# Optimization experiments

Measured on AMD Instinct MI355X. Metric: run time of the kernel, lower is better.

The kernel has to match this reference:

```python
import jax, jax.numpy as jnp
import numpy as np

T, B, S, H, E, V = 16, 32, 256, 256, 300, 1000


def setup_inputs() -> dict:
    key = jax.random.key(0)
    ks = jax.random.split(key, 16)
    p = lambda k, shp: (jax.random.normal(k, shp, dtype=jnp.float32) * 0.05)
    return {
        "target_variable": jax.random.randint(ks[0], (T, B), 0, V),
        "h0": p(ks[1], (1, B, H)),
        "c0": p(ks[2], (1, B, H)),
        "encoder_outputs": jax.random.normal(ks[3], (S, B, H), dtype=jnp.float32),
        "encoder_lens": jax.random.randint(ks[4], (B,), 1, S + 1),
        "embedding": p(ks[5], (V, E)),
        "W_ih": p(ks[6], (4 * H, E)),
        "W_hh": p(ks[7], (4 * H, H)),
        "b_ih": p(ks[8], (4 * H,)),
        "b_hh": p(ks[9], (4 * H,)),
        "We": p(ks[10], (H, H)),
        "be": p(ks[11], (H,)),
        "Wd": p(ks[12], (H, H)),
        "bd": p(ks[13], (H,)),
        "wa": p(ks[14], (H,)),
        "ba": p(ks[14], (1,)),
        "W_out": p(ks[15], (V, 2 * H)),
        "b_out": p(ks[15], (V,)),
    }


def _lstm(x, h0, c0, W_ih, W_hh, b_ih, b_hh):
    # x: [T,B,E]; torch gate order i,f,g,o
    x_proj = jnp.einsum('tbe,ge->tbg', x, W_ih) + b_ih  # [T,B,4H]
    def step(carry, xg):
        h, c = carry
        g = xg + h @ W_hh.T + b_hh
        i, f, gg, o = jnp.split(g, 4, axis=-1)
        c = jax.nn.sigmoid(f) * c + jax.nn.sigmoid(i) * jnp.tanh(gg)
        h = jax.nn.sigmoid(o) * jnp.tanh(c)
        return (h, c), h
    (hT, cT), outs = jax.lax.scan(step, (h0[0], c0[0]), x_proj)
    return outs, hT[None], cT[None]


def reference(target_variable, h0, c0, encoder_outputs, encoder_lens,
              embedding, W_ih, W_hh, b_ih, b_hh,
              We, be, Wd, bd, wa, ba, W_out, b_out):
    emb = embedding[target_variable]                      # [T,B,E] (dropout p=0 -> identity)
    output, hT, cT = _lstm(emb, h0, c0, W_ih, W_hh, b_ih, b_hh)  # output [T,B,H]
    # additive attention: same math as expand+Linear, applied before broadcast
    enc_t = jnp.einsum('sbh,gh->sbg', encoder_outputs, We) + be   # [S,B,H]
    dec_t = jnp.einsum('tbh,gh->tbg', output, Wd) + bd            # [T,B,H]
    scores = jnp.einsum('tsbh,h->tsb', jnp.tanh(enc_t[None, :, :, :] + dec_t[:, None, :, :]), wa) + ba[0]
    raw_attention = jnp.transpose(scores, (2, 0, 1))              # [B,T,S]
    valid = (jnp.arange(S)[None, None, :] < encoder_lens[:, None, None])  # [B,1,S]
    raw_attention = jnp.where(valid, raw_attention, -jnp.inf)
    attention = jax.nn.softmax(raw_attention, axis=2)             # [B,T,S]
    enc_bf = jnp.transpose(encoder_outputs, (1, 0, 2))            # [B,S,H]
    context = jnp.einsum('bts,bsh->bth', attention, enc_bf)       # [B,T,H]
    out_bf = jnp.transpose(output, (1, 0, 2))                     # [B,T,H]
    combined = jnp.transpose(jnp.concatenate([context, out_bf], axis=2), (1, 0, 2))  # [T,B,2H]
    logits = jnp.einsum('tbh,vh->tbv', combined, W_out) + b_out
    output_prob = jax.nn.softmax(logits, axis=2)                  # [T,B,V]
    return output_prob, hT, cT, context
```

## Files before the change

kernel.cpp:

```cpp
#include <hip/hip_runtime.h>
#include <hip/hip_fp16.h>
#include <math.h>

typedef unsigned int u32;
typedef unsigned short u16;

#define T_ 16
#define B_ 32
#define S_ 256
#define H_ 256
#define E_ 300
#define V_ 1000

typedef _Float16 h2_t __attribute__((ext_vector_type(2)));
typedef __fp16  fp16v2 __attribute__((ext_vector_type(2)));

__device__ __forceinline__ float fast_tanh(float x) {
    return 1.0f - 2.0f / (__expf(2.0f * x) + 1.0f);
}
__device__ __forceinline__ float fast_sigm(float x) {
    return 1.0f / (1.0f + __expf(-x));
}
__device__ __forceinline__ float bf2f(u16 x) { return __uint_as_float(((u32)x) << 16); }
__device__ __forceinline__ float blo(u32 u) { return __uint_as_float(u << 16); }
__device__ __forceinline__ float bhi(u32 u) { return __uint_as_float(u & 0xffff0000u); }
__device__ __forceinline__ u16 f2bf(float f) {
    u32 u = __float_as_uint(f);
    u32 r = (u + 0x7fffu + ((u >> 16) & 1u)) >> 16;
    return (u16)r;
}
__device__ __forceinline__ h2_t u2h2(u32 u) {
    union { u32 a; h2_t b; } c; c.a = u; return c.b;
}
__device__ __forceinline__ u32 pk2(float a, float b) {
    union { fp16v2 v; u32 u; } c; c.v = __builtin_amdgcn_cvt_pkrtz(a, b); return c.u;
}
__device__ __forceinline__ float dot2f16(u32 w, u32 h, float acc) {
#if __has_builtin(__builtin_amdgcn_fdot2)
    return __builtin_amdgcn_fdot2(u2h2(w), u2h2(h), acc, false);
#else
    h2_t wv = u2h2(w), hv = u2h2(h);
    return acc + (float)wv.x * (float)hv.x + (float)wv.y * (float)hv.y;
#endif
}

__device__ void gemm_tile_256(const float* __restrict__ A, const int* __restrict__ gidx,
                              int lda, const float* __restrict__ Bw,
                              const float* __restrict__ bias, float* __restrict__ C,
                              int N, int K, int ldc, int bm, int bn)
{
    __shared__ float As[32][64];
    __shared__ float Bs[32][64];
    const int tid = threadIdx.x;
    const int ty = tid >> 4, tx = tid & 15;
    const int lr = tid >> 2;
    const int lk = (tid & 3) * 8;

    int am = bm + lr;
    int arow = gidx ? gidx[am] : am;
    const float* Ap = A + (size_t)arow * lda;
    int bnr = bn + lr;
    const float* Bp = (bnr < N) ? (Bw + (size_t)bnr * K) : nullptr;

    float acc[4][4] = {};

    for (int k0 = 0; k0 < K; k0 += 32) {
        int kb = k0 + lk;
        float av[8];
        if (kb + 8 <= K) {
            float4 p0 = *(const float4*)(Ap + kb);
            float4 p1 = *(const float4*)(Ap + kb + 4);
            av[0]=p0.x; av[1]=p0.y; av[2]=p0.z; av[3]=p0.w;
            av[4]=p1.x; av[5]=p1.y; av[6]=p1.z; av[7]=p1.w;
        } else {
            #pragma unroll
            for (int j = 0; j < 8; j++) av[j] = (kb + j < K) ? Ap[kb + j] : 0.0f;
        }
        #pragma unroll
        for (int j = 0; j < 8; j++) As[lk + j][lr] = av[j];
        if (Bp && kb + 8 <= K) {
            float4 p0 = *(const float4*)(Bp + kb);
            float4 p1 = *(const float4*)(Bp + kb + 4);
            av[0]=p0.x; av[1]=p0.y; av[2]=p0.z; av[3]=p0.w;
            av[4]=p1.x; av[5]=p1.y; av[6]=p1.z; av[7]=p1.w;
        } else if (Bp) {
            #pragma unroll
            for (int j = 0; j < 8; j++) av[j] = (kb + j < K) ? Bp[kb + j] : 0.0f;
        } else {
            #pragma unroll
            for (int j = 0; j < 8; j++) av[j] = 0.0f;
        }
        #pragma unroll
        for (int j = 0; j < 8; j++) Bs[lk + j][lr] = av[j];
        __syncthreads();
        #pragma unroll
        for (int kk = 0; kk < 32; kk++) {
            float4 a = *(const float4*)&As[kk][ty * 4];
            float4 b = *(const float4*)&Bs[kk][tx * 4];
            acc[0][0] += a.x*b.x; acc[0][1] += a.x*b.y; acc[0][2] += a.x*b.z; acc[0][3] += a.x*b.w;
            acc[1][0] += a.y*b.x; acc[1][1] += a.y*b.y; acc[1][2] += a.y*b.z; acc[1][3] += a.y*b.w;
            acc[2][0] += a.z*b.x; acc[2][1] += a.z*b.y; acc[2][2] += a.z*b.z; acc[2][3] += a.z*b.w;
            acc[3][0] += a.w*b.x; acc[3][1] += a.w*b.y; acc[3][2] += a.w*b.z; acc[3][3] += a.w*b.w;
        }
        __syncthreads();
    }
    #pragma unroll
    for (int i = 0; i < 4; i++) {
        int m = bm + ty * 4 + i;
        #pragma unroll
        for (int j = 0; j < 4; j++) {
            int n = bn + tx * 4 + j;
            if (n < N) C[(size_t)m * ldc + n] = acc[i][j] + bias[n];
        }
    }
}

__global__ __launch_bounds__(256)
void prep_xproj(const float* __restrict__ emb, const int* __restrict__ tv,
                const float* __restrict__ W_ih, const float* __restrict__ b_ih,
                float* __restrict__ xproj,
                const float* __restrict__ Whh,  u32* __restrict__ Wt2,
                const float* __restrict__ Wd,   float* __restrict__ Wdt,
                const float* __restrict__ W_out, u16* __restrict__ WoTb)
{
    const int bid = blockIdx.x;
    if (bid < 128) {
        gemm_tile_256(emb, tv, E_, W_ih, b_ih, xproj, 1024, E_, 1024,
                      (bid >> 4) * 64, (bid & 15) * 64);
        return;
    }
    __shared__ float tile[64][65];
    const int tid = threadIdx.x;
    const int wv = tid >> 6;
    const int lane = tid & 63;

    if (bid < 192) {
        int t = bid - 128;
        int r0 = (t >> 2) * 64, k0 = (t & 3) * 64;
        #pragma unroll 4
        for (int j = 0; j < 16; j++) {
            int row = wv * 16 + j;
            tile[row][lane] = Whh[(size_t)(r0 + row) * 256 + k0 + lane];
        }
        __syncthreads();
        #pragma unroll
        for (int it = 0; it < 2; it++) {
            int q = wv + 4 * it;
            uint4 val;
            val.x = pk2(tile[lane][8*q + 0], tile[lane][8*q + 1]);
            val.y = pk2(tile[lane][8*q + 2], tile[lane][8*q + 3]);
            val.z = pk2(tile[lane][8*q + 4], tile[lane][8*q + 5]);
            val.w = pk2(tile[lane][8*q + 6], tile[lane][8*q + 7]);
            ((uint4*)Wt2)[(size_t)((k0 >> 3) + q) * 1024 + r0 + lane] = val;
        }
    } else if (bid < 208) {
        int t = bid - 192;
        int h0 = (t >> 2) * 64, k0 = (t & 3) * 64;
        #pragma unroll 4
        for (int j = 0; j < 16; j++) {
            int row = wv * 16 + j;
            tile[row][lane] = Wd[(size_t)(h0 + row) * 256 + k0 + lane];
        }
        __syncthreads();
        #pragma unroll
        for (int it = 0; it < 4; it++) {
            int q = wv + 4 * it;
            float4 v;
            v.x = tile[lane][4*q + 0];
            v.y = tile[lane][4*q + 1];
            v.z = tile[lane][4*q + 2];
            v.w = tile[lane][4*q + 3];
            ((float4*)Wdt)[(size_t)((k0 >> 2) + q) * 256 + h0 + lane] = v;
        }
    } else {
        int t = bid - 208;
        int v0 = (t >> 3) * 64, k0 = (t & 7) * 64;
        #pragma unroll 4
        for (int j = 0; j < 16; j++) {
            int row = wv * 16 + j;
            int v = v0 + row;
            tile[row][lane] = (v < V_) ? W_out[(size_t)v * 512 + k0 + lane] : 0.0f;
        }
        __syncthreads();
        #pragma unroll
        for (int it = 0; it < 4; it++) {
            int q = wv + 4 * it;
            int v = v0 + lane;
            float a0 = tile[lane][4*q + 0], a1 = tile[lane][4*q + 1];
            float a2 = tile[lane][4*q + 2], a3 = tile[lane][4*q + 3];
            float b0 = __shfl_xor(a0, 1, 64), b1 = __shfl_xor(a1, 1, 64);
            float b2 = __shfl_xor(a2, 1, 64), b3 = __shfl_xor(a3, 1, 64);
            if (!(lane & 1) && v < V_) {
                uint4 w;
                w.x = (u32)f2bf(a0) | ((u32)f2bf(b0) << 16);
                w.y = (u32)f2bf(a1) | ((u32)f2bf(b1) << 16);
                w.z = (u32)f2bf(a2) | ((u32)f2bf(b2) << 16);
                w.w = (u32)f2bf(a3) | ((u32)f2bf(b3) << 16);
                ((uint4*)WoTb)[(size_t)((k0 >> 2) + q) * 500 + (v >> 1)] = w;
            }
        }
    }
}

__global__ __launch_bounds__(1024, 4)
void lstm_enct(const float* __restrict__ xproj,
               const u32*   __restrict__ Wt2,
               const float* __restrict__ bhh,
               const float* __restrict__ h0, const float* __restrict__ c0,
               float* __restrict__ combined,
               float* __restrict__ hT, float* __restrict__ cT,
               const float* __restrict__ enc_raw,
               const float* __restrict__ We,
               const float* __restrict__ be,
               float* __restrict__ enct)
{
    const int bid = blockIdx.x;
    const int tid = threadIdx.x;
    __shared__ __align__(16) u32 smem[34176];

    if (bid < 32) {
        float* zs = (float*)smem;
        float* cs = (float*)(smem + 1024);
        u32*   hp = smem + 1280;
        u32*   wlds = smem + 1408;
        const int b = bid;
        const int r = tid;
        if (tid < 256) {
            float h0v = h0[b * 256 + tid];
            cs[tid] = c0[b * 256 + tid];
            float hpart = __shfl_xor(h0v, 1, 64);
            if (!(tid & 1)) hp[tid >> 1] = pk2(h0v, hpart);
        }
        const float bh = bhh[r];
        const uint4* wp4 = (const uint4*)Wt2 + r;

        uint4 wreg[16];
        #pragma unroll
        for (int j = 0; j < 16; j++) wreg[j] = wp4[(size_t)(16 + j) * 1024];
        #pragma unroll
        for (int j = 0; j < 8; j++) {
            uint4 w = wp4[(size_t)(8 + j) * 1024];
            wlds[(j * 4 + 0) * 1024 + r] = w.x;
            wlds[(j * 4 + 1) * 1024 + r] = w.y;
            wlds[(j * 4 + 2) * 1024 + r] = w.z;
            wlds[(j * 4 + 3) * 1024 + r] = w.w;
        }
        __syncthreads();

        for (int t = 0; t < T_; t++) {
            float xp = xproj[((size_t)t * B_ + b) * 1024 + r];
            float acc = 0.0f;
            const uint4* hp4 = (const uint4*)hp;
            #pragma unroll
            for (int i = 0; i < 8; i++) {
                uint4 hv = hp4[i];
                uint4 w  = wp4[(size_t)i * 1024];
                acc = dot2f16(w.x, hv.x, acc);
                acc = dot2f16(w.y, hv.y, acc);
                acc = dot2f16(w.z, hv.z, acc);
                acc = dot2f16(w.w, hv.w, acc);
            }
            #pragma unroll
            for (int j = 0; j < 8; j++) {
                uint4 hv = hp4[8 + j];
                u32 w0 = wlds[(j * 4 + 0) * 1024 + r];
                u32 w1 = wlds[(j * 4 + 1) * 1024 + r];
                u32 w2 = wlds[(j * 4 + 2) * 1024 + r];
                u32 w3 = wlds[(j * 4 + 3) * 1024 + r];
                acc = dot2f16(w0, hv.x, acc);
                acc = dot2f16(w1, hv.y, acc);
                acc = dot2f16(w2, hv.z, acc);
                acc = dot2f16(w3, hv.w, acc);
            }
            #pragma unroll
            for (int j = 0; j < 16; j++) {
                uint4 hv = hp4[16 + j];
                acc = dot2f16(wreg[j].x, hv.x, acc);
                acc = dot2f16(wreg[j].y, hv.y, acc);
                acc = dot2f16(wreg[j].z, hv.z, acc);
                acc = dot2f16(wreg[j].w, hv.w, acc);
            }
            zs[r] = xp + bh + acc;
            __syncthreads();

            if (tid < 256) {
                float ig = fast_sigm(zs[tid]);
                float fg = fast_sigm(zs[256 + tid]);
                float gg = fast_tanh(zs[512 + tid]);
                float og = fast_sigm(zs[768 + tid]);
                float c = fg * cs[tid] + ig * gg;
                float h = og * fast_tanh(c);
                cs[tid] = c;
                combined[((size_t)t * B_ + b) * 512 + 256 + tid] = h;
                if (t == T_ - 1) {
                    hT[b * 256 + tid] = h;
                    cT[b * 256 + tid] = c;
                }
                float hpart = __shfl_xor(h, 1, 64);
                if (!(tid & 1)) hp[tid >> 1] = pk2(h, hpart);
            }
            __syncthreads();
        }
    } else {
        float (*As2)[132] = (float (*)[132])smem;
        float (*Bs2)[132] = (float (*)[132])(smem + 4224);
        const int tile = bid - 32;
        const int bm = (tile >> 1) * 128;
        const int bn = (tile & 1) * 128;
        const int tx = tid & 31, ty = tid >> 5;
        const int lr = tid >> 3;
        const int lk = (tid & 7) * 4;

        const float* Ap = enc_raw + (size_t)(bm + lr) * 256;
        const float* Bp = We + (size_t)(bn + lr) * 256;
        float acc[4][4] = {};

        for (int k0 = 0; k0 < 256; k0 += 32) {
            float4 a4 = *(const float4*)(Ap + k0 + lk);
            float4 b4 = *(const float4*)(Bp + k0 + lk);
            As2[lk + 0][lr] = a4.x; As2[lk + 1][lr] = a4.y;
            As2[lk + 2][lr] = a4.z; As2[lk + 3][lr] = a4.w;
            Bs2[lk + 0][lr] = b4.x; Bs2[lk + 1][lr] = b4.y;
            Bs2[lk + 2][lr] = b4.z; Bs2[lk + 3][lr] = b4.w;
            __syncthreads();
            #pragma unroll
            for (int kk = 0; kk < 32; kk++) {
                float4 a = *(const float4*)&As2[kk][ty * 4];
                float4 b = *(const float4*)&Bs2[kk][tx * 4];
                acc[0][0] += a.x*b.x; acc[0][1] += a.x*b.y; acc[0][2] += a.x*b.z; acc[0][3] += a.x*b.w;
                acc[1][0] += a.y*b.x; acc[1][1] += a.y*b.y; acc[1][2] += a.y*b.z; acc[1][3] += a.y*b.w;
                acc[2][0] += a.z*b.x; acc[2][1] += a.z*b.y; acc[2][2] += a.z*b.z; acc[2][3] += a.z*b.w;
                acc[3][0] += a.w*b.x; acc[3][1] += a.w*b.y; acc[3][2] += a.w*b.z; acc[3][3] += a.w*b.w;
            }
            __syncthreads();
        }
        #pragma unroll
        for (int i = 0; i < 4; i++) {
            int m = bm + ty * 4 + i;
            #pragma unroll
            for (int j = 0; j < 4; j++) {
                int n = bn + tx * 4 + j;
                enct[(size_t)m * 256 + n] = acc[i][j] + be[n];
            }
        }
    }
}

__global__ __launch_bounds__(512)
void attn_logits(const float* __restrict__ enct,
                 const float* __restrict__ combined_in,
                 const float* __restrict__ Wdt,
                 const float* __restrict__ bd,
                 const float* __restrict__ enc_raw,
                 const float* __restrict__ wa, const float* __restrict__ ba,
                 const int* __restrict__ lens,
                 const u16* __restrict__ WoTb,
                 const float* __restrict__ b_out,
                 float* __restrict__ ctx_out,
                 float* __restrict__ probs)
{
    const int bid = blockIdx.x;
    const int b = bid & 31;
    const int t = bid >> 5;
    const int tid = threadIdx.x;
    const int wv = tid >> 6, lane = tid & 63;
    __shared__ float ds[256], was[256], sc[256];
    __shared__ float crow[512];
    __shared__ float tmp2[512];
    __shared__ float lrow[1000];
    __shared__ float red[8], red2[8];

    if (tid < 256) {
        crow[256 + tid] = combined_in[((size_t)t * B_ + b) * 512 + 256 + tid];
        was[tid] = wa[tid];
    }
    const int len = lens[b];
    const float bav = ba[0];
    __syncthreads();

    {
        const int h   = tid & 255;
        const int kq0 = (tid >> 8) * 32;
        float acc = 0.0f;
        const float4* wp = (const float4*)Wdt + h;
        #pragma unroll 8
        for (int kq = kq0; kq < kq0 + 32; kq++) {
            float4 w = wp[(size_t)kq * 256];
            float4 c = *(const float4*)&crow[256 + kq * 4];
            acc += w.x * c.x;
            acc += w.y * c.y;
            acc += w.z * c.z;
            acc += w.w * c.w;
        }
        tmp2[tid] = acc;
    }
    __syncthreads();
    if (tid < 256) ds[tid] = bd[tid] + tmp2[tid] + tmp2[tid + 256];
    __syncthreads();

    for (int s = wv; s < len; s += 8) {
        const float* er = enct + ((size_t)s * B_ + b) * 256;
        float sum = 0.0f;
        #pragma unroll
        for (int j = 0; j < 4; j++) {
            int h = lane + 64 * j;
            sum += fast_tanh(er[h] + ds[h]) * was[h];
        }
        #pragma unroll
        for (int off = 32; off >= 1; off >>= 1) sum += __shfl_xor(sum, off, 64);
        if (lane == 0) sc[s] = sum + bav;
    }
    __syncthreads();

    float x = (tid < len) ? sc[tid] : -INFINITY;
    float m = x;
    #pragma unroll
    for (int off = 32; off >= 1; off >>= 1) m = fmaxf(m, __shfl_xor(m, off, 64));
    if (lane == 0) red[wv] = m;
    __syncthreads();
    m = red[0];
    #pragma unroll
    for (int i = 1; i < 8; i++) m = fmaxf(m, red[i]);
    float e = __expf(x - m);
    float ssum = e;
    #pragma unroll
    for (int off = 32; off >= 1; off >>= 1) ssum += __shfl_xor(ssum, off, 64);
    if (lane == 0) red2[wv] = ssum;
    __syncthreads();
    ssum = red2[0] + red2[1] + red2[2] + red2[3] + red2[4] + red2[5] + red2[6] + red2[7];
    if (tid < 256) sc[tid] = e / ssum;
    __syncthreads();

    {
        const int h  = tid & 255;
        const int sg = tid >> 8;
        const int mid = (len + 1) >> 1;
        const int s0 = sg ? mid : 0;
        const int s1 = sg ? len : mid;
        float cacc = 0.0f;
        const float* eb = enc_raw + (size_t)b * 256 + h;
        #pragma unroll 4
        for (int s = s0; s < s1; s++) cacc += sc[s] * eb[(size_t)s * (B_ * H_)];
        tmp2[tid] = cacc;
    }
    __syncthreads();
    if (tid < 256) {
        float ctx = tmp2[tid] + tmp2[tid + 256];
        ctx_out[((size_t)b * T_ + t) * 256 + tid] = ctx;
        crow[tid] = ctx;
    }
    __syncthreads();

    if (tid < 500) {
        const int v0 = tid * 2;
        float a0 = b_out[v0], a1 = b_out[v0 + 1];
        const uint4* wp = (const uint4*)WoTb + tid;
        #pragma unroll 8
        for (int kq = 0; kq < 128; kq++) {
            uint4 w = wp[(size_t)kq * 500];
            float4 c = *(const float4*)&crow[kq * 4];
            a0 += c.x * blo(w.x); a1 += c.x * bhi(w.x);
            a0 += c.y * blo(w.y); a1 += c.y * bhi(w.y);
            a0 += c.z * blo(w.z); a1 += c.z * bhi(w.z);
            a0 += c.w * blo(w.w); a1 += c.w * bhi(w.w);
        }
        lrow[v0] = a0;
        lrow[v0 + 1] = a1;
    }
    __syncthreads();

    float v0v = -INFINITY, v1v = -INFINITY;
    if (tid < 500) { v0v = lrow[tid * 2]; v1v = lrow[tid * 2 + 1]; }
    float mx = fmaxf(v0v, v1v);
    #pragma unroll
    for (int off = 32; off >= 1; off >>= 1) mx = fmaxf(mx, __shfl_xor(mx, off, 64));
    if (lane == 0) red[wv] = mx;
    __syncthreads();
    mx = red[0];
    #pragma unroll
    for (int i = 1; i < 8; i++) mx = fmaxf(mx, red[i]);
    float e0 = __expf(v0v - mx), e1 = __expf(v1v - mx);
    float s2 = e0 + e1;
    #pragma unroll
    for (int off = 32; off >= 1; off >>= 1) s2 += __shfl_xor(s2, off, 64);
    if (lane == 0) red2[wv] = s2;
    __syncthreads();
    s2 = red2[0] + red2[1] + red2[2] + red2[3] + red2[4] + red2[5] + red2[6] + red2[7];
    float inv = 1.0f / s2;
    if (tid < 500) {
        float2 pv = make_float2(e0 * inv, e1 * inv);
        *(float2*)&probs[((size_t)t * B_ + b) * V_ + tid * 2] = pv;
    }
}

extern "C" void kernel_launch(void* const* d_in, const int* in_sizes, int n_in,
                              void* d_out, int out_size, void* d_ws, size_t ws_size,
                              hipStream_t stream) {
    const int*   tv       = (const int*)d_in[0];
    const float* h0       = (const float*)d_in[1];
    const float* c0       = (const float*)d_in[2];
    const float* enc_raw  = (const float*)d_in[3];
    const int*   lens     = (const int*)d_in[4];
    const float* emb      = (const float*)d_in[5];
    const float* W_ih     = (const float*)d_in[6];
    const float* W_hh     = (const float*)d_in[7];
    const float* b_ih     = (const float*)d_in[8];
    const float* b_hh     = (const float*)d_in[9];
    const float* We       = (const float*)d_in[10];
    const float* be       = (const float*)d_in[11];
    const float* Wd       = (const float*)d_in[12];
    const float* bd       = (const float*)d_in[13];
    const float* wa       = (const float*)d_in[14];
    const float* ba       = (const float*)d_in[15];
    const float* W_out    = (const float*)d_in[16];
    const float* b_out    = (const float*)d_in[17];

    float* ws       = (float*)d_ws;
    float* enct     = ws;
    float* xproj    = ws + 2097152;
    float* Wdt      = ws + 2621440;
    u16*   WoTb     = (u16*)(ws + 2752512);
    float* combined = ws + 3264512;
    u32*   Wt2      = (u32*)(ws + 3526656);

    float* out      = (float*)d_out;
    float* probs    = out;
    float* hT       = out + 512000;
    float* cT       = out + 520192;
    float* ctx_out  = out + 528384;

    prep_xproj<<<336, 256, 0, stream>>>(emb, tv, W_ih, b_ih, xproj,
                                        W_hh, Wt2, Wd, Wdt, W_out, WoTb);
    lstm_enct<<<160, 1024, 0, stream>>>(xproj, Wt2, b_hh, h0, c0, combined, hT, cT,
                                        enc_raw, We, be, enct);
    attn_logits<<<512, 512, 0, stream>>>(enct, combined, Wdt, bd, enc_raw,
                                         wa, ba, lens, WoTb, b_out, ctx_out, probs);
}
```

Before: 213.3 us.

## Process two timesteps per attention block and prefetch next xproj in LSTM

The attention/logits kernel now handles two decoder timesteps per block, halving the grid to 256 blocks. Each load of Wdt, enct, encoder outputs and the bf16 W_out is reused for both timesteps, roughly halving weight and encoder traffic. Separately, the LSTM loop loads the next step's input projection one iteration early to hide its latency behind the recurrent dot product. The cost is lower parallelism (256 blocks on a large GPU), more registers and shared memory per block, and extra barriers in the per-timestep softmax loops.

Result: slower. 223.2 us (+4.7%).

```diff
diff --git a/kernel.cpp b/kernel.cpp
--- a/kernel.cpp
+++ b/kernel.cpp
@@ -247,8 +247,9 @@
         }
         __syncthreads();
 
+        float xp = xproj[(size_t)b * 1024 + r];
         for (int t = 0; t < T_; t++) {
-            float xp = xproj[((size_t)t * B_ + b) * 1024 + r];
+            float xp_next = (t + 1 < T_) ? xproj[((size_t)(t + 1) * B_ + b) * 1024 + r] : 0.0f;
             float acc = 0.0f;
             const uint4* hp4 = (const uint4*)hp;
             #pragma unroll
@@ -300,6 +301,7 @@
                 if (!(tid & 1)) hp[tid >> 1] = pk2(h, hpart);
             }
             __syncthreads();
+            xp = xp_next;
         }
     } else {
         float (*As2)[132] = (float (*)[132])smem;
@@ -361,17 +363,19 @@
 {
     const int bid = blockIdx.x;
     const int b = bid & 31;
-    const int t = bid >> 5;
+    const int tp = bid >> 5;
+    const int t0 = tp * 2, t1 = t0 + 1;
     const int tid = threadIdx.x;
     const int wv = tid >> 6, lane = tid & 63;
-    __shared__ float ds[256], was[256], sc[256];
-    __shared__ float crow[512];
-    __shared__ float tmp2[512];
-    __shared__ float lrow[1000];
+    __shared__ float ds[2][256], was[256], sc[2][256];
+    __shared__ float crow[2][512];
+    __shared__ float tmp2[2][512];
+    __shared__ float lrow[2][1000];
     __shared__ float red[8], red2[8];
 
     if (tid < 256) {
-        crow[256 + tid] = combined_in[((size_t)t * B_ + b) * 512 + 256 + tid];
+        crow[0][256 + tid] = combined_in[((size_t)t0 * B_ + b) * 512 + 256 + tid];
+        crow[1][256 + tid] = combined_in[((size_t)t1 * B_ + b) * 512 + 256 + tid];
         was[tid] = wa[tid];
     }
     const int len = lens[b];
@@ -381,55 +385,65 @@
     {
         const int h   = tid & 255;
         const int kq0 = (tid >> 8) * 32;
-        float acc = 0.0f;
+        float a0 = 0.0f, a1 = 0.0f;
         const float4* wp = (const float4*)Wdt + h;
-        #pragma unroll 8
+        #pragma unroll 4
         for (int kq = kq0; kq < kq0 + 32; kq++) {
             float4 w = wp[(size_t)kq * 256];
-            float4 c = *(const float4*)&crow[256 + kq * 4];
-            acc += w.x * c.x;
-            acc += w.y * c.y;
-            acc += w.z * c.z;
-            acc += w.w * c.w;
-        }
-        tmp2[tid] = acc;
-    }
-    __syncthreads();
-    if (tid < 256) ds[tid] = bd[tid] + tmp2[tid] + tmp2[tid + 256];
+            float4 c0v = *(const float4*)&crow[0][256 + kq * 4];
+            float4 c1v = *(const float4*)&crow[1][256 + kq * 4];
+            a0 += w.x * c0v.x; a0 += w.y * c0v.y; a0 += w.z * c0v.z; a0 += w.w * c0v.w;
+            a1 += w.x * c1v.x; a1 += w.y * c1v.y; a1 += w.z * c1v.z; a1 += w.w * c1v.w;
+        }
+        tmp2[0][tid] = a0;
+        tmp2[1][tid] = a1;
+    }
+    __syncthreads();
+    if (tid < 256) {
+        ds[0][tid] = bd[tid] + tmp2[0][tid] + tmp2[0][tid + 256];
+        ds[1][tid] = bd[tid] + tmp2[1][tid] + tmp2[1][tid + 256];
+    }
     __syncthreads();
 
     for (int s = wv; s < len; s += 8) {
         const float* er = enct + ((size_t)s * B_ + b) * 256;
-        float sum = 0.0f;
+        float sum0 = 0.0f, sum1 = 0.0f;
         #pragma unroll
         for (int j = 0; j < 4; j++) {
             int h = lane + 64 * j;
-            sum += fast_tanh(er[h] + ds[h]) * was[h];
-        }
-        #pragma unroll
-        for (int off = 32; off >= 1; off >>= 1) sum += __shfl_xor(sum, off, 64);
-        if (lane == 0) sc[s] = sum + bav;
-    }
-    __syncthreads();
-
-    float x = (tid < len) ? sc[tid] : -INFINITY;
-    float m = x;
+            float ev = er[h];
+            sum0 += fast_tanh(ev + ds[0][h]) * was[h];
+            sum1 += fast_tanh(ev + ds[1][h]) * was[h];
+        }
+        #pragma unroll
+        for (int off = 32; off >= 1; off >>= 1) sum0 += __shfl_xor(sum0, off, 64);
+        #pragma unroll
+        for (int off = 32; off >= 1; off >>= 1) sum1 += __shfl_xor(sum1, off, 64);
+        if (lane == 0) { sc[0][s] = sum0 + bav; sc[1][s] = sum1 + bav; }
+    }
+    __syncthreads();
+
     #pragma unroll
-    for (int off = 32; off >= 1; off >>= 1) m = fmaxf(m, __shfl_xor(m, off, 64));
-    if (lane == 0) red[wv] = m;
-    __syncthreads();
-    m = red[0];
-    #pragma unroll
-    for (int i = 1; i < 8; i++) m = fmaxf(m, red[i]);
-    float e = __expf(x - m);
-    float ssum = e;
-    #pragma unroll
-    for (int off = 32; off >= 1; off >>= 1) ssum += __shfl_xor(ssum, off, 64);
-    if (lane == 0) red2[wv] = ssum;
-    __syncthreads();
-    ssum = red2[0] + red2[1] + red2[2] + red2[3] + red2[4] + red2[5] + red2[6] + red2[7];
-    if (tid < 256) sc[tid] = e / ssum;
-    __syncthreads();
+    for (int ti = 0; ti < 2; ti++) {
+        float x = (tid < len) ? sc[ti][tid] : -INFINITY;
+        float m = x;
+        #pragma unroll
+        for (int off = 32; off >= 1; off >>= 1) m = fmaxf(m, __shfl_xor(m, off, 64));
+        if (lane == 0) red[wv] = m;
+        __syncthreads();
+        m = red[0];
+        #pragma unroll
+        for (int i = 1; i < 8; i++) m = fmaxf(m, red[i]);
+        float e = __expf(x - m);
+        float ssum = e;
+        #pragma unroll
+        for (int off = 32; off >= 1; off >>= 1) ssum += __shfl_xor(ssum, off, 64);
+        if (lane == 0) red2[wv] = ssum;
+        __syncthreads();
+        ssum = red2[0] + red2[1] + red2[2] + red2[3] + red2[4] + red2[5] + red2[6] + red2[7];
+        if (tid < 256) sc[ti][tid] = e / ssum;
+        __syncthreads();
+    }
 
     {
         const int h  = tid & 255;
@@ -437,59 +451,83 @@
         const int mid = (len + 1) >> 1;
         const int s0 = sg ? mid : 0;
         const int s1 = sg ? len : mid;
-        float cacc = 0.0f;
+        float c0a = 0.0f, c1a = 0.0f;
         const float* eb = enc_raw + (size_t)b * 256 + h;
         #pragma unroll 4
-        for (int s = s0; s < s1; s++) cacc += sc[s] * eb[(size_t)s * (B_ * H_)];
-        tmp2[tid] = cacc;
+        for (int s = s0; s < s1; s++) {
+            float ev = eb[(size_t)s * (B_ * H_)];
+            c0a += sc[0][s] * ev;
+            c1a += sc[1][s] * ev;
+        }
+        tmp2[0][tid] = c0a;
+        tmp2[1][tid] = c1a;
     }
     __syncthreads();
     if (tid < 256) {
-        float ctx = tmp2[tid] + tmp2[tid + 256];
-        ctx_out[((size_t)b * T_ + t) * 256 + tid] = ctx;
-        crow[tid] = ctx;
+        float ctx0 = tmp2[0][tid] + tmp2[0][tid + 256];
+        float ctx1 = tmp2[1][tid] + tmp2[1][tid + 256];
+        ctx_out[((size_t)b * T_ + t0) * 256 + tid] = ctx0;
+        ctx_out[((size_t)b * T_ + t1) * 256 + tid] = ctx1;
+        crow[0][tid] = ctx0;
+        crow[1][tid] = ctx1;
     }
     __syncthreads();
 
     if (tid < 500) {
         const int v0 = tid * 2;
-        float a0 = b_out[v0], a1 = b_out[v0 + 1];
+        const float b0v = b_out[v0], b1v = b_out[v0 + 1];
+        float a00 = b0v, a01 = b1v;
+        float a10 = b0v, a11 = b1v;
         const uint4* wp = (const uint4*)WoTb + tid;
-        #pragma unroll 8
+        #pragma unroll 4
         for (int kq = 0; kq < 128; kq++) {
             uint4 w = wp[(size_t)kq * 500];
-            float4 c = *(const float4*)&crow[kq * 4];
-            a0 += c.x * blo(w.x); a1 += c.x * bhi(w.x);
-            a0 += c.y * blo(w.y); a1 += c.y * bhi(w.y);
-            a0 += c.z * blo(w.z); a1 += c.z * bhi(w.z);
-            a0 += c.w * blo(w.w); a1 += c.w * bhi(w.w);
-        }
-        lrow[v0] = a0;
-        lrow[v0 + 1] = a1;
-    }
-    __syncthreads();
-
-    float v0v = -INFINITY, v1v = -INFINITY;
-    if (tid < 500) { v0v = lrow[tid * 2]; v1v = lrow[tid * 2 + 1]; }
-    float mx = fmaxf(v0v, v1v);
+            float4 c0v = *(const float4*)&crow[0][kq * 4];
+            float4 c1v = *(const float4*)&crow[1][kq * 4];
+            float wxl = blo(w.x), wxh = bhi(w.x);
+            float wyl = blo(w.y), wyh = bhi(w.y);
+            float wzl = blo(w.z), wzh = bhi(w.z);
+            float wwl = blo(w.w), wwh = bhi(w.w);
+            a00 += c0v.x * wxl; a01 += c0v.x * wxh;
+            a00 += c0v.y * wyl; a01 += c0v.y * wyh;
+            a00 += c0v.z * wzl; a01 += c0v.z * wzh;
+            a00 += c0v.w * wwl; a01 += c0v.w * wwh;
+            a10 += c1v.x * wxl; a11 += c1v.x * wxh;
+            a10 += c1v.y * wyl; a11 += c1v.y * wyh;
+            a10 += c1v.z * wzl; a11 += c1v.z * wzh;
+            a10 += c1v.w * wwl; a11 += c1v.w * wwh;
+        }
+        lrow[0][v0] = a00; lrow[0][v0 + 1] = a01;
+        lrow[1][v0] = a10; lrow[1][v0 + 1] = a11;
+    }
+    __syncthreads();
+
     #pragma unroll
-    for (int off = 32; off >= 1; off >>= 1) mx = fmaxf(mx, __shfl_xor(mx, off, 64));
-    if (lane == 0) red[wv] = mx;
-    __syncthreads();
-    mx = red[0];
-    #pragma unroll
-    for (int i = 1; i < 8; i++) mx = fmaxf(mx, red[i]);
-    float e0 = __expf(v0v - mx), e1 = __expf(v1v - mx);
-    float s2 = e0 + e1;
-    #pragma unroll
-    for (int off = 32; off >= 1; off >>= 1) s2 += __shfl_xor(s2, off, 64);
-    if (lane == 0) red2[wv] = s2;
-    __syncthreads();
-    s2 = red2[0] + red2[1] + red2[2] + red2[3] + red2[4] + red2[5] + red2[6] + red2[7];
-    float inv = 1.0f / s2;
-    if (tid < 500) {
-        float2 pv = make_float2(e0 * inv, e1 * inv);
-        *(float2*)&probs[((size_t)t * B_ + b) * V_ + tid * 2] = pv;
+    for (int ti = 0; ti < 2; ti++) {
+        const int tt = t0 + ti;
+        float v0v = -INFINITY, v1v = -INFINITY;
+        if (tid < 500) { v0v = lrow[ti][tid * 2]; v1v = lrow[ti][tid * 2 + 1]; }
+        float mx = fmaxf(v0v, v1v);
+        #pragma unroll
+        for (int off = 32; off >= 1; off >>= 1) mx = fmaxf(mx, __shfl_xor(mx, off, 64));
+        if (lane == 0) red[wv] = mx;
+        __syncthreads();
+        mx = red[0];
+        #pragma unroll
+        for (int i = 1; i < 8; i++) mx = fmaxf(mx, red[i]);
+        float e0 = __expf(v0v - mx), e1 = __expf(v1v - mx);
+        float s2 = e0 + e1;
+        #pragma unroll
+        for (int off = 32; off >= 1; off >>= 1) s2 += __shfl_xor(s2, off, 64);
+        if (lane == 0) red2[wv] = s2;
+        __syncthreads();
+        s2 = red2[0] + red2[1] + red2[2] + red2[3] + red2[4] + red2[5] + red2[6] + red2[7];
+        float inv = 1.0f / s2;
+        if (tid < 500) {
+            float2 pv = make_float2(e0 * inv, e1 * inv);
+            *(float2*)&probs[((size_t)tt * B_ + b) * V_ + tid * 2] = pv;
+        }
+        __syncthreads();
     }
 }
 
@@ -533,6 +571,6 @@
                                         W_hh, Wt2, Wd, Wdt, W_out, WoTb);
     lstm_enct<<<160, 1024, 0, stream>>>(xproj, Wt2, b_hh, h0, c0, combined, hT, cT,
                                         enc_raw, We, be, enct);
-    attn_logits<<<512, 512, 0, stream>>>(enct, combined, Wdt, bd, enc_raw,
+    attn_logits<<<256, 512, 0, stream>>>(enct, combined, Wdt, bd, enc_raw,
                                          wa, ba, lens, WoTb, b_out, ctx_out, probs);
 }
```
